# Kernel optimization log

Hardware: AMD Instinct MI355X
Metric: run time of the kernel (lower is better)

Reference implementation:

```python
import jax, jax.numpy as jnp
import numpy as np

D_MODEL = 1024
NUM_HEADS = 16
HEAD_DIM = D_MODEL // NUM_HEADS
D_FF = 4096
B, S = 4, 2048
EPS = 1e-5


def layernorm(x, gamma, beta):
    mu = jnp.mean(x, axis=-1, keepdims=True)
    var = jnp.mean(jnp.square(x - mu), axis=-1, keepdims=True)
    return (x - mu) * jax.lax.rsqrt(var + EPS) * gamma + beta


def setup_inputs() -> dict:
    key = jax.random.key(0)
    ks = jax.random.split(key, 16)
    s_in = 1.0 / np.sqrt(D_MODEL)
    s_ff = 1.0 / np.sqrt(D_FF)
    return {
        "x": jax.random.normal(ks[0], (B, S, D_MODEL), jnp.float32),
        "Wq": jax.random.normal(ks[1], (D_MODEL, D_MODEL), jnp.float32) * s_in,
        "bq": jnp.zeros((D_MODEL,), jnp.float32),
        "Wk": jax.random.normal(ks[2], (D_MODEL, D_MODEL), jnp.float32) * s_in,
        "bk": jnp.zeros((D_MODEL,), jnp.float32),
        "Wv": jax.random.normal(ks[3], (D_MODEL, D_MODEL), jnp.float32) * s_in,
        "bv": jnp.zeros((D_MODEL,), jnp.float32),
        "Wo": jax.random.normal(ks[4], (D_MODEL, D_MODEL), jnp.float32) * s_in,
        "bo": jnp.zeros((D_MODEL,), jnp.float32),
        "W1": jax.random.normal(ks[5], (D_MODEL, D_FF), jnp.float32) * s_in,
        "b1": jnp.zeros((D_FF,), jnp.float32),
        "W2": jax.random.normal(ks[6], (D_FF, D_MODEL), jnp.float32) * s_ff,
        "b2": jnp.zeros((D_MODEL,), jnp.float32),
        "g1": jnp.ones((D_MODEL,), jnp.float32),
        "be1": jnp.zeros((D_MODEL,), jnp.float32),
        "g2": jnp.ones((D_MODEL,), jnp.float32),
        "be2": jnp.zeros((D_MODEL,), jnp.float32),
    }


def reference(x, Wq, bq, Wk, bk, Wv, bv, Wo, bo, W1, b1, W2, b2, g1, be1, g2, be2):
    # multi-head self-attention (dropout is identity at eval)
    def split_heads(t):  # [B,S,D] -> [B,H,S,hd]
        return t.reshape(B, S, NUM_HEADS, HEAD_DIM).transpose(0, 2, 1, 3)

    q = split_heads(x @ Wq + bq)
    k = split_heads(x @ Wk + bk)
    v = split_heads(x @ Wv + bv)
    scores = jnp.einsum("bhqd,bhkd->bhqk", q, k) / np.sqrt(HEAD_DIM)
    attn = jax.nn.softmax(scores, axis=-1)
    out = jnp.einsum("bhqk,bhkd->bhqd", attn, v)
    out = out.transpose(0, 2, 1, 3).reshape(B, S, D_MODEL)
    attn_out = out @ Wo + bo

    h = layernorm(x + attn_out, g1, be1)
    ff = jax.nn.relu(h @ W1 + b1) @ W2 + b2
    return layernorm(h + ff, g2, be2)
```

## Files before the change

kernel.cpp:

```cpp
#include <hip/hip_runtime.h>
#include <hip/hip_bf16.h>


#define DM    1024
#define DFF   4096
#define NH    16
#define HD    64
#define BATCH 4
#define SEQ   2048
#define TOK   (BATCH * SEQ)

typedef __attribute__((ext_vector_type(8))) __bf16 bf16x8;
typedef __attribute__((ext_vector_type(4))) float f32x4;
typedef __attribute__((ext_vector_type(4))) unsigned short u16x4;

typedef const __attribute__((address_space(1))) unsigned int* gas1_t;
typedef __attribute__((address_space(3))) unsigned int* las3_t;

__device__ __forceinline__ void gl_lds16(const void* g, void* l) {
  __builtin_amdgcn_global_load_lds((gas1_t)g, (las3_t)l, 16, 0, 0);
}

__device__ __forceinline__ unsigned short f2bu(float x) {
  return __builtin_bit_cast(unsigned short, __float2bfloat16(x));
}

__global__ __launch_bounds__(256) void cast_bf16(
    const float* __restrict__ in, unsigned short* __restrict__ out, int n4) {
  int i = blockIdx.x * 256 + threadIdx.x;
  if (i >= n4) return;
  float4 v = ((const float4*)in)[i];
  u16x4 o = {f2bu(v.x), f2bu(v.y), f2bu(v.z), f2bu(v.w)};
  ((u16x4*)out)[i] = o;
}

__global__ __launch_bounds__(256) void transpose_cast(
    const float* __restrict__ in, unsigned short* __restrict__ out, int K, int N) {
  __shared__ float tile[32][33];
  int n0 = blockIdx.x * 32, k0 = blockIdx.y * 32;
  int tx = threadIdx.x, ty = threadIdx.y;
#pragma unroll
  for (int i = 0; i < 4; ++i)
    tile[ty + 8 * i][tx] = in[(size_t)(k0 + ty + 8 * i) * N + n0 + tx];
  __syncthreads();
#pragma unroll
  for (int i = 0; i < 4; ++i)
    out[(size_t)(n0 + ty + 8 * i) * K + k0 + tx] = f2bu(tile[tx][ty + 8 * i]);
}

__device__ __forceinline__ void gemm_mainloop(
    const unsigned short* __restrict__ A, const unsigned short* __restrict__ Bt,
    int K, int m0, int n0, unsigned short* As, unsigned short* Bs,
    f32x4 acc[4][4]) {
  const int tid = threadIdx.x, lane = tid & 63, w = tid >> 6;
  const int l15 = lane & 15, quad = lane >> 4;
  const int wr = w >> 1, wc = w & 1;

  int rowS[2], colS[2];
#pragma unroll
  for (int i = 0; i < 2; ++i) {
    int f16 = (i * 4 + w) * 64 + lane;
    rowS[i] = f16 >> 2;
    colS[i] = ((f16 & 3) ^ (rowS[i] & 3)) * 8;
  }
  const int swz = (quad ^ (l15 & 3)) * 16;

  for (int kb = 0; kb < K; kb += 32) {
#pragma unroll
    for (int i = 0; i < 2; ++i) {
      gl_lds16(A + (size_t)(m0 + rowS[i]) * K + kb + colS[i],
               (char*)As + (size_t)((i * 4 + w) * 1024));
      gl_lds16(Bt + (size_t)(n0 + rowS[i]) * K + kb + colS[i],
               (char*)Bs + (size_t)((i * 4 + w) * 1024));
    }
    __syncthreads();
    bf16x8 aF[4], bF[4];
#pragma unroll
    for (int t = 0; t < 4; ++t) {
      aF[t] = *(const bf16x8*)((const char*)As + (wr * 64 + t * 16 + l15) * 64 + swz);
      bF[t] = *(const bf16x8*)((const char*)Bs + (wc * 64 + t * 16 + l15) * 64 + swz);
    }
#pragma unroll
    for (int mi = 0; mi < 4; ++mi)
#pragma unroll
      for (int ni = 0; ni < 4; ++ni)
        acc[mi][ni] = __builtin_amdgcn_mfma_f32_16x16x32_bf16(
            aF[mi], bF[ni], acc[mi][ni], 0, 0, 0);
    __syncthreads();
  }
}

__global__ __launch_bounds__(256) void gemm_bt(
    const unsigned short* __restrict__ A, const unsigned short* __restrict__ Bt,
    const float* __restrict__ bias, void* __restrict__ Cout,
    int N, int K, float alpha, int relu, int ofp32) {
  __shared__ unsigned short As[128 * 32];
  __shared__ unsigned short Bs[128 * 32];
  const int tid = threadIdx.x, lane = tid & 63, w = tid >> 6;
  const int l15 = lane & 15, quad = lane >> 4;
  const int m0 = blockIdx.y * 128, n0 = blockIdx.x * 128;
  const int wr = w >> 1, wc = w & 1;

  f32x4 acc[4][4];
#pragma unroll
  for (int mi = 0; mi < 4; ++mi)
#pragma unroll
    for (int ni = 0; ni < 4; ++ni) acc[mi][ni] = {0.f, 0.f, 0.f, 0.f};

  gemm_mainloop(A, Bt, K, m0, n0, As, Bs, acc);

#pragma unroll
  for (int ni = 0; ni < 4; ++ni) {
    int col = n0 + wc * 64 + ni * 16 + l15;
    float bvv = bias[col];
#pragma unroll
    for (int mi = 0; mi < 4; ++mi) {
      int rbase = m0 + wr * 64 + mi * 16 + quad * 4;
#pragma unroll
      for (int r = 0; r < 4; ++r) {
        float val = alpha * (acc[mi][ni][r] + bvv);
        if (relu) val = fmaxf(val, 0.f);
        size_t idx = (size_t)(rbase + r) * N + col;
        if (ofp32) ((float*)Cout)[idx] = val;
        else ((unsigned short*)Cout)[idx] = f2bu(val);
      }
    }
  }
}

__global__ __launch_bounds__(256) void gemm_qkv(
    const unsigned short* __restrict__ A, const unsigned short* __restrict__ Bt,
    const float* __restrict__ bq, const float* __restrict__ bk,
    const float* __restrict__ bv,
    unsigned short* __restrict__ Qb, unsigned short* __restrict__ Kb,
    unsigned short* __restrict__ Vtg) {
  __shared__ unsigned short As[128 * 32];
  __shared__ unsigned short Bs[128 * 32];
  const int tid = threadIdx.x, lane = tid & 63, w = tid >> 6;
  const int l15 = lane & 15, quad = lane >> 4;
  const int m0 = blockIdx.y * 128, n0 = blockIdx.x * 128;
  const int wr = w >> 1, wc = w & 1;

  f32x4 acc[4][4];
#pragma unroll
  for (int mi = 0; mi < 4; ++mi)
#pragma unroll
    for (int ni = 0; ni < 4; ++ni) acc[mi][ni] = {0.f, 0.f, 0.f, 0.f};

  gemm_mainloop(A, Bt, DM, m0, n0, As, Bs, acc);

  const int region = n0 >> 10;
  const int nloc0 = (n0 & 1023) + wc * 64;
  if (region < 2) {
    unsigned short* Out = region ? Kb : Qb;
    const float* bias = region ? bk : bq;
    const float alpha = region ? 1.0f : 0.125f;
#pragma unroll
    for (int ni = 0; ni < 4; ++ni) {
      int col = nloc0 + ni * 16 + l15;
      float bvv = bias[col];
#pragma unroll
      for (int mi = 0; mi < 4; ++mi) {
        int rbase = m0 + wr * 64 + mi * 16 + quad * 4;
#pragma unroll
        for (int r = 0; r < 4; ++r)
          Out[(size_t)(rbase + r) * DM + col] = f2bu(alpha * (acc[mi][ni][r] + bvv));
      }
    }
  } else {
#pragma unroll
    for (int ni = 0; ni < 4; ++ni) {
      int col = nloc0 + ni * 16 + l15;
      float bvv = bv[col];
      int hh = col >> 6, dl = col & 63;
#pragma unroll
      for (int mi = 0; mi < 4; ++mi) {
        int rbase = m0 + wr * 64 + mi * 16 + quad * 4;
        int b_ = rbase >> 11, s0 = rbase & 2047;
        u16x4 pk;
#pragma unroll
        for (int r = 0; r < 4; ++r) pk[r] = f2bu(acc[mi][ni][r] + bvv);
        *(u16x4*)(Vtg + ((size_t)((b_ * NH + hh) * HD + dl)) * SEQ + s0) = pk;
      }
    }
  }
}

__global__ __launch_bounds__(256) void attn_kernel(
    const unsigned short* __restrict__ Q, const unsigned short* __restrict__ K,
    const unsigned short* __restrict__ Vtg, unsigned short* __restrict__ O) {
  __shared__ unsigned short Kt[64 * 64];
  __shared__ unsigned short Vt[64 * 64];
  __shared__ unsigned short Pt[4][16 * 64];
  __shared__ __align__(16) float redA[4][16];
  __shared__ __align__(16) float redL[4][16];

  const int tid = threadIdx.x, lane = tid & 63, w = tid >> 6;
  const int l15 = lane & 15, quad = lane >> 4;
  const int q0 = blockIdx.x * 64;
  const int bh = blockIdx.y, b = bh >> 4, hh = bh & 15;
  const size_t tokbase = (size_t)b * SEQ;

  bf16x8 qf[2];
#pragma unroll
  for (int kk = 0; kk < 2; ++kk)
    qf[kk] = *(const bf16x8*)(Q + (tokbase + q0 + w * 16 + l15) * DM + hh * HD +
                              kk * 32 + quad * 8);

  float m_run = -3.0e38f, l_run = 0.f;
  f32x4 Oacc[4];
#pragma unroll
  for (int nt = 0; nt < 4; ++nt) Oacc[nt] = {0.f, 0.f, 0.f, 0.f};

  char* ptw = (char*)&Pt[w][0];

  for (int j = 0; j < SEQ / 64; ++j) {
    const int kv0 = j * 64;
    __syncthreads();
#pragma unroll
    for (int i = 0; i < 2; ++i) {
      int f = (i * 4 + w) * 64 + lane;
      int row = f >> 3, csrc = (f & 7) ^ (row & 7);
      gl_lds16(K + (tokbase + kv0 + row) * DM + hh * HD + csrc * 8,
               (char*)Kt + (size_t)(i * 4 + w) * 1024);
      gl_lds16(Vtg + ((size_t)bh * HD + row) * SEQ + kv0 + csrc * 8,
               (char*)Vt + (size_t)(i * 4 + w) * 1024);
    }
    __syncthreads();

    f32x4 S[4];
#pragma unroll
    for (int mt = 0; mt < 4; ++mt) S[mt] = {0.f, 0.f, 0.f, 0.f};
#pragma unroll
    for (int kk = 0; kk < 2; ++kk) {
#pragma unroll
      for (int mt = 0; mt < 4; ++mt) {
        int row = mt * 16 + l15;
        bf16x8 aK = *(const bf16x8*)((const char*)Kt + row * 128 +
                                     (((kk * 4 + quad) ^ (row & 7)) * 16));
        S[mt] = __builtin_amdgcn_mfma_f32_16x16x32_bf16(aK, qf[kk], S[mt], 0, 0, 0);
      }
    }

    float mx = S[0][0];
#pragma unroll
    for (int mt = 0; mt < 4; ++mt)
#pragma unroll
      for (int r = 0; r < 4; ++r) mx = fmaxf(mx, S[mt][r]);
    mx = fmaxf(mx, __shfl_xor(mx, 16));
    mx = fmaxf(mx, __shfl_xor(mx, 32));
    float mn = fmaxf(m_run, mx);
    float al = __expf(m_run - mn);
    m_run = mn;
    float rs = 0.f;
#pragma unroll
    for (int mt = 0; mt < 4; ++mt) {
      u16x4 pk;
#pragma unroll
      for (int r = 0; r < 4; ++r) {
        float p = __expf(S[mt][r] - mn);
        rs += p;
        pk[r] = f2bu(p);
      }
      *(u16x4*)(ptw + l15 * 128 +
                (((mt * 2 + (quad >> 1)) ^ (l15 & 7)) * 16 + (quad & 1) * 8)) = pk;
    }
    rs += __shfl_xor(rs, 16);
    rs += __shfl_xor(rs, 32);
    l_run = l_run * al + rs;
    if (lane < 16) redA[w][lane] = al;
    f32x4 alv = *(const f32x4*)&redA[w][quad * 4];
#pragma unroll
    for (int nt = 0; nt < 4; ++nt) Oacc[nt] *= alv;

#pragma unroll
    for (int kk = 0; kk < 2; ++kk) {
      bf16x8 aP = *(const bf16x8*)(ptw + l15 * 128 +
                                   (((kk * 4 + quad) ^ (l15 & 7)) * 16));
#pragma unroll
      for (int nt = 0; nt < 4; ++nt) {
        int row = nt * 16 + l15;
        bf16x8 bV = *(const bf16x8*)((const char*)Vt + row * 128 +
                                     (((kk * 4 + quad) ^ (row & 7)) * 16));
        Oacc[nt] = __builtin_amdgcn_mfma_f32_16x16x32_bf16(aP, bV, Oacc[nt], 0, 0, 0);
      }
    }
  }

  if (lane < 16) redL[w][lane] = l_run;
  f32x4 lv = *(const f32x4*)&redL[w][quad * 4];
  f32x4 li;
#pragma unroll
  for (int r = 0; r < 4; ++r) li[r] = 1.0f / lv[r];
#pragma unroll
  for (int nt = 0; nt < 4; ++nt)
#pragma unroll
    for (int r = 0; r < 4; ++r) {
      size_t tok = tokbase + q0 + w * 16 + quad * 4 + r;
      O[tok * DM + hh * HD + nt * 16 + l15] = f2bu(Oacc[nt][r] * li[r]);
    }
}

__global__ __launch_bounds__(256) void ln_res(
    const float* __restrict__ base, const float* __restrict__ delta,
    const float* __restrict__ gamma, const float* __restrict__ beta,
    float* __restrict__ outf, unsigned short* __restrict__ outb) {
  __shared__ float red[8];
  const int row = blockIdx.x, tid = threadIdx.x;
  const size_t rb = (size_t)row * DM;
  float4 xv = ((const float4*)(base + rb))[tid];
  float4 dv = ((const float4*)(delta + rb))[tid];
  float s0 = xv.x + dv.x, s1 = xv.y + dv.y, s2 = xv.z + dv.z, s3 = xv.w + dv.w;
  float t = s0 + s1 + s2 + s3;
#pragma unroll
  for (int m = 1; m < 64; m <<= 1) t += __shfl_xor(t, m);
  if ((tid & 63) == 0) red[tid >> 6] = t;
  __syncthreads();
  float mu = (red[0] + red[1] + red[2] + red[3]) * (1.0f / DM);
  float d0 = s0 - mu, d1 = s1 - mu, d2 = s2 - mu, d3 = s3 - mu;
  float v = d0 * d0 + d1 * d1 + d2 * d2 + d3 * d3;
#pragma unroll
  for (int m = 1; m < 64; m <<= 1) v += __shfl_xor(v, m);
  if ((tid & 63) == 0) red[4 + (tid >> 6)] = v;
  __syncthreads();
  float var = (red[4] + red[5] + red[6] + red[7]) * (1.0f / DM);
  float rs = rsqrtf(var + 1e-5f);
  float4 gv = ((const float4*)gamma)[tid];
  float4 bv = ((const float4*)beta)[tid];
  float o0 = d0 * rs * gv.x + bv.x;
  float o1 = d1 * rs * gv.y + bv.y;
  float o2 = d2 * rs * gv.z + bv.z;
  float o3 = d3 * rs * gv.w + bv.w;
  float4 ov = {o0, o1, o2, o3};
  ((float4*)(outf + rb))[tid] = ov;
  if (outb) {
    u16x4 ob = {f2bu(o0), f2bu(o1), f2bu(o2), f2bu(o3)};
    ((u16x4*)(outb + rb))[tid] = ob;
  }
}

extern "C" void kernel_launch(void* const* d_in, const int* in_sizes, int n_in,
                              void* d_out, int out_size, void* d_ws, size_t ws_size,
                              hipStream_t stream) {
  const float* x   = (const float*)d_in[0];
  const float* Wq  = (const float*)d_in[1];  const float* bq  = (const float*)d_in[2];
  const float* Wk  = (const float*)d_in[3];  const float* bk  = (const float*)d_in[4];
  const float* Wv  = (const float*)d_in[5];  const float* bvv = (const float*)d_in[6];
  const float* Wo  = (const float*)d_in[7];  const float* bo  = (const float*)d_in[8];
  const float* W1  = (const float*)d_in[9];  const float* b1  = (const float*)d_in[10];
  const float* W2  = (const float*)d_in[11]; const float* b2  = (const float*)d_in[12];
  const float* g1  = (const float*)d_in[13]; const float* be1 = (const float*)d_in[14];
  const float* g2  = (const float*)d_in[15]; const float* be2 = (const float*)d_in[16];

  char* ws = (char*)d_ws;
  const size_t MB = 1ull << 20;
  unsigned short* xb    = (unsigned short*)(ws + 0 * MB);
  unsigned short* wqkvT = (unsigned short*)(ws + 16 * MB);
  unsigned short* woT   = (unsigned short*)(ws + 22 * MB);
  unsigned short* w1T   = (unsigned short*)(ws + 24 * MB);
  unsigned short* w2T   = (unsigned short*)(ws + 32 * MB);
  unsigned short* Qb    = (unsigned short*)(ws + 40 * MB);
  unsigned short* Kb    = (unsigned short*)(ws + 56 * MB);
  unsigned short* Vtg   = (unsigned short*)(ws + 72 * MB);
  unsigned short* aO    = (unsigned short*)(ws + 104 * MB);
  float*          prj   = (float*)(ws + 120 * MB);
  float*          h     = (float*)(ws + 152 * MB);
  unsigned short* hb    = (unsigned short*)(ws + 0 * MB);
  unsigned short* ffm   = (unsigned short*)(ws + 40 * MB);
  float*          ffo   = (float*)(ws + 104 * MB);
  (void)ws_size; (void)in_sizes; (void)n_in; (void)out_size;

  cast_bf16<<<TOK * DM / 4 / 256, 256, 0, stream>>>(x, xb, TOK * DM / 4);
  transpose_cast<<<dim3(DM / 32, DM / 32), dim3(32, 8), 0, stream>>>(Wq, wqkvT, DM, DM);
  transpose_cast<<<dim3(DM / 32, DM / 32), dim3(32, 8), 0, stream>>>(Wk, wqkvT + 1024 * 1024, DM, DM);
  transpose_cast<<<dim3(DM / 32, DM / 32), dim3(32, 8), 0, stream>>>(Wv, wqkvT + 2048 * 1024, DM, DM);
  transpose_cast<<<dim3(DM / 32, DM / 32), dim3(32, 8), 0, stream>>>(Wo, woT, DM, DM);
  transpose_cast<<<dim3(DFF / 32, DM / 32), dim3(32, 8), 0, stream>>>(W1, w1T, DM, DFF);
  transpose_cast<<<dim3(DM / 32, DFF / 32), dim3(32, 8), 0, stream>>>(W2, w2T, DFF, DM);

  gemm_qkv<<<dim3(3 * DM / 128, TOK / 128), 256, 0, stream>>>(
      xb, wqkvT, bq, bk, bvv, Qb, Kb, Vtg);

  attn_kernel<<<dim3(SEQ / 64, BATCH * NH), 256, 0, stream>>>(Qb, Kb, Vtg, aO);

  gemm_bt<<<dim3(DM / 128, TOK / 128), 256, 0, stream>>>(aO, woT, bo, prj, DM, DM, 1.0f, 0, 1);
  ln_res<<<TOK, 256, 0, stream>>>(x, prj, g1, be1, h, hb);

  gemm_bt<<<dim3(DFF / 128, TOK / 128), 256, 0, stream>>>(hb, w1T, b1, ffm, DFF, DM, 1.0f, 1, 0);
  gemm_bt<<<dim3(DM / 128, TOK / 128), 256, 0, stream>>>(ffm, w2T, b2, ffo, DM, DFF, 1.0f, 0, 1);

  ln_res<<<TOK, 256, 0, stream>>>(h, ffo, g2, be2, (float*)d_out, nullptr);
}
```

Before: 640.3 us.

## Double-buffer attention K/V tiles, process 32 queries per wave, use exp2

The attention kernel now gives each wave two 16-query groups, so every K/V fragment read from LDS feeds two MFMAs, which halves the block count and the K/V reloads. K/V tiles are double-buffered so the next tile's global-to-LDS load overlaps compute, removing one barrier per iteration. Q is pre-scaled by log2(e)/8 so softmax can use the hardware exp2 instead of expf. The four 1024x1024 weight transpose-casts are merged into one launch. Risks include higher register and LDS use lowering occupancy, and only 1024 attention blocks to spread across the CUs.

```diff
diff --git a/kernel.cpp b/kernel.cpp
--- a/kernel.cpp
+++ b/kernel.cpp
@@ -46,6 +46,30 @@
 #pragma unroll
   for (int i = 0; i < 4; ++i)
     out[(size_t)(n0 + ty + 8 * i) * K + k0 + tx] = f2bu(tile[tx][ty + 8 * i]);
+}
+
+__global__ __launch_bounds__(256) void transpose_cast4(
+    const float* __restrict__ A0, const float* __restrict__ A1,
+    const float* __restrict__ A2, const float* __restrict__ A3,
+    unsigned short* __restrict__ O0, unsigned short* __restrict__ O1,
+    unsigned short* __restrict__ O2, unsigned short* __restrict__ O3) {
+  __shared__ float tile[32][33];
+  const float* in; unsigned short* out;
+  switch (blockIdx.z) {
+    case 0: in = A0; out = O0; break;
+    case 1: in = A1; out = O1; break;
+    case 2: in = A2; out = O2; break;
+    default: in = A3; out = O3; break;
+  }
+  int n0 = blockIdx.x * 32, k0 = blockIdx.y * 32;
+  int tx = threadIdx.x, ty = threadIdx.y;
+#pragma unroll
+  for (int i = 0; i < 4; ++i)
+    tile[ty + 8 * i][tx] = in[(size_t)(k0 + ty + 8 * i) * DM + n0 + tx];
+  __syncthreads();
+#pragma unroll
+  for (int i = 0; i < 4; ++i)
+    out[(size_t)(n0 + ty + 8 * i) * DM + k0 + tx] = f2bu(tile[tx][ty + 8 * i]);
 }
 
 __device__ __forceinline__ void gemm_mainloop(
@@ -127,6 +151,8 @@
     }
   }
 }
+
+#define QSCALE 0.18033688f
 
 __global__ __launch_bounds__(256) void gemm_qkv(
     const unsigned short* __restrict__ A, const unsigned short* __restrict__ Bt,
@@ -154,7 +180,7 @@
   if (region < 2) {
     unsigned short* Out = region ? Kb : Qb;
     const float* bias = region ? bk : bq;
-    const float alpha = region ? 1.0f : 0.125f;
+    const float alpha = region ? 1.0f : QSCALE;
 #pragma unroll
     for (int ni = 0; ni < 4; ++ni) {
       int col = nloc0 + ni * 16 + l15;
@@ -189,116 +215,152 @@
 __global__ __launch_bounds__(256) void attn_kernel(
     const unsigned short* __restrict__ Q, const unsigned short* __restrict__ K,
     const unsigned short* __restrict__ Vtg, unsigned short* __restrict__ O) {
-  __shared__ unsigned short Kt[64 * 64];
-  __shared__ unsigned short Vt[64 * 64];
-  __shared__ unsigned short Pt[4][16 * 64];
-  __shared__ __align__(16) float redA[4][16];
-  __shared__ __align__(16) float redL[4][16];
+  __shared__ unsigned short Kt[2][64 * 64];
+  __shared__ unsigned short Vt[2][64 * 64];
+  __shared__ unsigned short Pt[4][32 * 64];
+  __shared__ __align__(16) float redA[4][32];
+  __shared__ __align__(16) float redL[4][32];
 
   const int tid = threadIdx.x, lane = tid & 63, w = tid >> 6;
   const int l15 = lane & 15, quad = lane >> 4;
-  const int q0 = blockIdx.x * 64;
+  const int q0 = blockIdx.x * 128;
   const int bh = blockIdx.y, b = bh >> 4, hh = bh & 15;
   const size_t tokbase = (size_t)b * SEQ;
 
-  bf16x8 qf[2];
-#pragma unroll
-  for (int kk = 0; kk < 2; ++kk)
-    qf[kk] = *(const bf16x8*)(Q + (tokbase + q0 + w * 16 + l15) * DM + hh * HD +
-                              kk * 32 + quad * 8);
-
-  float m_run = -3.0e38f, l_run = 0.f;
-  f32x4 Oacc[4];
-#pragma unroll
-  for (int nt = 0; nt < 4; ++nt) Oacc[nt] = {0.f, 0.f, 0.f, 0.f};
+  bf16x8 qf[2][2];
+#pragma unroll
+  for (int qg = 0; qg < 2; ++qg)
+#pragma unroll
+    for (int kk = 0; kk < 2; ++kk)
+      qf[qg][kk] = *(const bf16x8*)(Q +
+          (tokbase + q0 + w * 32 + qg * 16 + l15) * DM + hh * HD + kk * 32 + quad * 8);
+
+  float m_run[2] = {-3.0e38f, -3.0e38f}, l_run[2] = {0.f, 0.f};
+  f32x4 Oacc[2][4];
+#pragma unroll
+  for (int qg = 0; qg < 2; ++qg)
+#pragma unroll
+    for (int nt = 0; nt < 4; ++nt) Oacc[qg][nt] = {0.f, 0.f, 0.f, 0.f};
 
   char* ptw = (char*)&Pt[w][0];
 
+  int rowS[2], csrcS[2];
+#pragma unroll
+  for (int i = 0; i < 2; ++i) {
+    int f = (i * 4 + w) * 64 + lane;
+    rowS[i] = f >> 3;
+    csrcS[i] = ((f & 7) ^ (rowS[i] & 7)) * 8;
+  }
+
+#define STAGE(jj, bb)                                                         \
+  {                                                                           \
+    const int kv0_ = (jj) * 64;                                               \
+    _Pragma("unroll") for (int i = 0; i < 2; ++i) {                           \
+      gl_lds16(K + (tokbase + kv0_ + rowS[i]) * DM + hh * HD + csrcS[i],      \
+               (char*)Kt[bb] + (size_t)((i * 4 + w) * 1024));                 \
+      gl_lds16(Vtg + ((size_t)bh * HD + rowS[i]) * SEQ + kv0_ + csrcS[i],     \
+               (char*)Vt[bb] + (size_t)((i * 4 + w) * 1024));                 \
+    }                                                                         \
+  }
+
+  STAGE(0, 0);
+
   for (int j = 0; j < SEQ / 64; ++j) {
-    const int kv0 = j * 64;
+    const int buf = j & 1;
     __syncthreads();
-#pragma unroll
-    for (int i = 0; i < 2; ++i) {
-      int f = (i * 4 + w) * 64 + lane;
-      int row = f >> 3, csrc = (f & 7) ^ (row & 7);
-      gl_lds16(K + (tokbase + kv0 + row) * DM + hh * HD + csrc * 8,
-               (char*)Kt + (size_t)(i * 4 + w) * 1024);
-      gl_lds16(Vtg + ((size_t)bh * HD + row) * SEQ + kv0 + csrc * 8,
-               (char*)Vt + (size_t)(i * 4 + w) * 1024);
-    }
-    __syncthreads();
-
-    f32x4 S[4];
-#pragma unroll
-    for (int mt = 0; mt < 4; ++mt) S[mt] = {0.f, 0.f, 0.f, 0.f};
+    if (j + 1 < SEQ / 64) STAGE(j + 1, buf ^ 1);
+
+    const char* ktb = (const char*)Kt[buf];
+    const char* vtb = (const char*)Vt[buf];
+
+    f32x4 S[2][4];
+#pragma unroll
+    for (int qg = 0; qg < 2; ++qg)
+#pragma unroll
+      for (int mt = 0; mt < 4; ++mt) S[qg][mt] = {0.f, 0.f, 0.f, 0.f};
 #pragma unroll
     for (int kk = 0; kk < 2; ++kk) {
 #pragma unroll
       for (int mt = 0; mt < 4; ++mt) {
-        int row = mt * 16 + l15;
-        bf16x8 aK = *(const bf16x8*)((const char*)Kt + row * 128 +
-                                     (((kk * 4 + quad) ^ (row & 7)) * 16));
-        S[mt] = __builtin_amdgcn_mfma_f32_16x16x32_bf16(aK, qf[kk], S[mt], 0, 0, 0);
-      }
-    }
-
-    float mx = S[0][0];
-#pragma unroll
-    for (int mt = 0; mt < 4; ++mt)
-#pragma unroll
-      for (int r = 0; r < 4; ++r) mx = fmaxf(mx, S[mt][r]);
-    mx = fmaxf(mx, __shfl_xor(mx, 16));
-    mx = fmaxf(mx, __shfl_xor(mx, 32));
-    float mn = fmaxf(m_run, mx);
-    float al = __expf(m_run - mn);
-    m_run = mn;
-    float rs = 0.f;
-#pragma unroll
-    for (int mt = 0; mt < 4; ++mt) {
-      u16x4 pk;
+        bf16x8 aK = *(const bf16x8*)(ktb + (mt * 16 + l15) * 128 +
+                                     (((kk * 4 + quad) ^ (l15 & 7)) * 16));
+        S[0][mt] = __builtin_amdgcn_mfma_f32_16x16x32_bf16(aK, qf[0][kk], S[0][mt], 0, 0, 0);
+        S[1][mt] = __builtin_amdgcn_mfma_f32_16x16x32_bf16(aK, qf[1][kk], S[1][mt], 0, 0, 0);
+      }
+    }
+
+#pragma unroll
+    for (int qg = 0; qg < 2; ++qg) {
+      float mx = S[qg][0][0];
+#pragma unroll
+      for (int mt = 0; mt < 4; ++mt)
+#pragma unroll
+        for (int r = 0; r < 4; ++r) mx = fmaxf(mx, S[qg][mt][r]);
+      mx = fmaxf(mx, __shfl_xor(mx, 16));
+      mx = fmaxf(mx, __shfl_xor(mx, 32));
+      float mn = fmaxf(m_run[qg], mx);
+      float al = __builtin_amdgcn_exp2f(m_run[qg] - mn);
+      m_run[qg] = mn;
+      float rs = 0.f;
+#pragma unroll
+      for (int mt = 0; mt < 4; ++mt) {
+        u16x4 pk;
+#pragma unroll
+        for (int r = 0; r < 4; ++r) {
+          float p = __builtin_amdgcn_exp2f(S[qg][mt][r] - mn);
+          rs += p;
+          pk[r] = f2bu(p);
+        }
+        *(u16x4*)(ptw + (qg * 16 + l15) * 128 +
+                  (((mt * 2 + (quad >> 1)) ^ (l15 & 7)) * 16 + (quad & 1) * 8)) = pk;
+      }
+      rs += __shfl_xor(rs, 16);
+      rs += __shfl_xor(rs, 32);
+      l_run[qg] = l_run[qg] * al + rs;
+      if (lane < 16) redA[w][qg * 16 + l15] = al;
+    }
+
+#pragma unroll
+    for (int qg = 0; qg < 2; ++qg) {
+      f32x4 alv = *(const f32x4*)&redA[w][qg * 16 + quad * 4];
+#pragma unroll
+      for (int nt = 0; nt < 4; ++nt) Oacc[qg][nt] *= alv;
+    }
+
+#pragma unroll
+    for (int kk = 0; kk < 2; ++kk) {
+      bf16x8 aP[2];
+#pragma unroll
+      for (int qg = 0; qg < 2; ++qg)
+        aP[qg] = *(const bf16x8*)(ptw + (qg * 16 + l15) * 128 +
+                                  (((kk * 4 + quad) ^ (l15 & 7)) * 16));
+#pragma unroll
+      for (int nt = 0; nt < 4; ++nt) {
+        bf16x8 bV = *(const bf16x8*)(vtb + (nt * 16 + l15) * 128 +
+                                     (((kk * 4 + quad) ^ (l15 & 7)) * 16));
+        Oacc[0][nt] = __builtin_amdgcn_mfma_f32_16x16x32_bf16(aP[0], bV, Oacc[0][nt], 0, 0, 0);
+        Oacc[1][nt] = __builtin_amdgcn_mfma_f32_16x16x32_bf16(aP[1], bV, Oacc[1][nt], 0, 0, 0);
+      }
+    }
+  }
+
+#pragma unroll
+  for (int qg = 0; qg < 2; ++qg)
+    if (lane < 16) redL[w][qg * 16 + l15] = l_run[qg];
+#pragma unroll
+  for (int qg = 0; qg < 2; ++qg) {
+    f32x4 lv = *(const f32x4*)&redL[w][qg * 16 + quad * 4];
+    f32x4 li;
+#pragma unroll
+    for (int r = 0; r < 4; ++r) li[r] = 1.0f / lv[r];
+#pragma unroll
+    for (int nt = 0; nt < 4; ++nt)
 #pragma unroll
       for (int r = 0; r < 4; ++r) {
-        float p = __expf(S[mt][r] - mn);
-        rs += p;
-        pk[r] = f2bu(p);
-      }
-      *(u16x4*)(ptw + l15 * 128 +
-                (((mt * 2 + (quad >> 1)) ^ (l15 & 7)) * 16 + (quad & 1) * 8)) = pk;
-    }
-    rs += __shfl_xor(rs, 16);
-    rs += __shfl_xor(rs, 32);
-    l_run = l_run * al + rs;
-    if (lane < 16) redA[w][lane] = al;
-    f32x4 alv = *(const f32x4*)&redA[w][quad * 4];
-#pragma unroll
-    for (int nt = 0; nt < 4; ++nt) Oacc[nt] *= alv;
-
-#pragma unroll
-    for (int kk = 0; kk < 2; ++kk) {
-      bf16x8 aP = *(const bf16x8*)(ptw + l15 * 128 +
-                                   (((kk * 4 + quad) ^ (l15 & 7)) * 16));
-#pragma unroll
-      for (int nt = 0; nt < 4; ++nt) {
-        int row = nt * 16 + l15;
-        bf16x8 bV = *(const bf16x8*)((const char*)Vt + row * 128 +
-                                     (((kk * 4 + quad) ^ (row & 7)) * 16));
-        Oacc[nt] = __builtin_amdgcn_mfma_f32_16x16x32_bf16(aP, bV, Oacc[nt], 0, 0, 0);
-      }
-    }
-  }
-
-  if (lane < 16) redL[w][lane] = l_run;
-  f32x4 lv = *(const f32x4*)&redL[w][quad * 4];
-  f32x4 li;
-#pragma unroll
-  for (int r = 0; r < 4; ++r) li[r] = 1.0f / lv[r];
-#pragma unroll
-  for (int nt = 0; nt < 4; ++nt)
-#pragma unroll
-    for (int r = 0; r < 4; ++r) {
-      size_t tok = tokbase + q0 + w * 16 + quad * 4 + r;
-      O[tok * DM + hh * HD + nt * 16 + l15] = f2bu(Oacc[nt][r] * li[r]);
-    }
+        size_t tok = tokbase + q0 + w * 32 + qg * 16 + quad * 4 + r;
+        O[tok * DM + hh * HD + nt * 16 + l15] = f2bu(Oacc[qg][nt][r] * li[r]);
+      }
+  }
 }
 
 __global__ __launch_bounds__(256) void ln_res(
@@ -371,17 +433,15 @@
   (void)ws_size; (void)in_sizes; (void)n_in; (void)out_size;
 
   cast_bf16<<<TOK * DM / 4 / 256, 256, 0, stream>>>(x, xb, TOK * DM / 4);
-  transpose_cast<<<dim3(DM / 32, DM / 32), dim3(32, 8), 0, stream>>>(Wq, wqkvT, DM, DM);
-  transpose_cast<<<dim3(DM / 32, DM / 32), dim3(32, 8), 0, stream>>>(Wk, wqkvT + 1024 * 1024, DM, DM);
-  transpose_cast<<<dim3(DM / 32, DM / 32), dim3(32, 8), 0, stream>>>(Wv, wqkvT + 2048 * 1024, DM, DM);
-  transpose_cast<<<dim3(DM / 32, DM / 32), dim3(32, 8), 0, stream>>>(Wo, woT, DM, DM);
+  transpose_cast4<<<dim3(DM / 32, DM / 32, 4), dim3(32, 8), 0, stream>>>(
+      Wq, Wk, Wv, Wo, wqkvT, wqkvT + 1024 * 1024, wqkvT + 2048 * 1024, woT);
   transpose_cast<<<dim3(DFF / 32, DM / 32), dim3(32, 8), 0, stream>>>(W1, w1T, DM, DFF);
   transpose_cast<<<dim3(DM / 32, DFF / 32), dim3(32, 8), 0, stream>>>(W2, w2T, DFF, DM);
 
   gemm_qkv<<<dim3(3 * DM / 128, TOK / 128), 256, 0, stream>>>(
       xb, wqkvT, bq, bk, bvv, Qb, Kb, Vtg);
 
-  attn_kernel<<<dim3(SEQ / 64, BATCH * NH), 256, 0, stream>>>(Qb, Kb, Vtg, aO);
+  attn_kernel<<<dim3(SEQ / 128, BATCH * NH), 256, 0, stream>>>(Qb, Kb, Vtg, aO);
 
   gemm_bt<<<dim3(DM / 128, TOK / 128), 256, 0, stream>>>(aO, woT, bo, prj, DM, DM, 1.0f, 0, 1);
   ln_res<<<TOK, 256, 0, stream>>>(x, prj, g1, be1, h, hb);
```

Result: no change. 645.9 us (+0.9%).
